# Performance work log

Hardware: AMD Instinct MI355X
Metric: run time of the kernel (lower is better)

The kernel has to match this reference:

```python
import jax, jax.numpy as jnp
import numpy as np

BETA = 0.25  # commitment loss coefficient


def setup_inputs() -> dict:
    key = jax.random.key(0)
    kx, kc = jax.random.split(key)
    # x: [B, T, D] latents; codebooks: [M, K, D] (equal K per level -> stacked)
    x = jax.random.normal(kx, (64, 1024, 256), dtype=jnp.float32)
    # small init akin to RandomUniform(-1/K, 1/K)
    codebooks = jax.random.normal(kc, (4, 1024, 256), dtype=jnp.float32) * (1.0 / 1024.0)
    return {"x": x, "codebooks": codebooks}


def reference(x, codebooks):
    """Residual VQ forward (inference path: no EMA state update).

    Returns (y, commit_loss): y = x + stop_grad(sum_l q_l - x) (straight-through),
    commit_loss = beta * sum_l mean((stop_grad(q_l) - r_l)^2).
    """
    D = x.shape[-1]
    M = codebooks.shape[0]
    flat = x.reshape(-1, D)                      # [N, D]
    residual = flat
    q_sum = jnp.zeros_like(flat)
    commit = jnp.zeros((), dtype=x.dtype)
    for lvl in range(M):                         # M is small & fixed (4)
        cb = codebooks[lvl]                      # [K, D]
        # squared L2 distances: ||r||^2 + ||e||^2 - 2 r.e^T
        r2 = jnp.sum(residual * residual, axis=1, keepdims=True)   # [N, 1]
        e2 = jnp.sum(cb * cb, axis=1)                               # [K]
        dist = r2 + e2 - 2.0 * jnp.matmul(residual, cb.T)           # [N, K]
        idx = jnp.argmin(dist, axis=1)                              # [N]
        q = jnp.take(cb, idx, axis=0)                               # [N, D]
        q_st = jax.lax.stop_gradient(q)
        commit = commit + BETA * jnp.mean((q_st - residual) ** 2)
        q_sum = q_sum + q
        residual = residual - q_st
    y_flat = flat + jax.lax.stop_gradient(q_sum - flat)
    return y_flat.reshape(x.shape), commit
```

## Files before the change

kernel.cpp:

```cpp
#include <hip/hip_runtime.h>

#define DIM 256
#define KCODES 1024
#define LEVELS 4
#define CHUNK 64
#define NCHUNK 16
#define TOKB 128
#define NTOK 65536
#define NELEM (NTOK * DIM)

typedef _Float16 h8 __attribute__((ext_vector_type(8)));
typedef _Float16 h4 __attribute__((ext_vector_type(4)));
typedef _Float16 h2 __attribute__((ext_vector_type(2)));
typedef float f4 __attribute__((ext_vector_type(4)));
typedef unsigned int u32;

__device__ __forceinline__ void gload16(const void* g, void* l) {
  __builtin_amdgcn_global_load_lds(
      (const __attribute__((address_space(1))) void*)g,
      (__attribute__((address_space(3))) void*)l, 16, 0, 0);
}

__device__ __forceinline__ float sq8(h8 r, float acc) {
#if __has_builtin(__builtin_amdgcn_fdot2)
  #pragma unroll
  for (int j = 0; j < 4; ++j) {
    h2 p = {r[2 * j], r[2 * j + 1]};
    acc = __builtin_amdgcn_fdot2(p, p, acc, false);
  }
#else
  #pragma unroll
  for (int j = 0; j < 8; ++j) { float v = (float)r[j]; acc += v * v; }
#endif
  return acc;
}

__global__ __launch_bounds__(256) void rvq_prep(const float* __restrict__ cb,
                                                _Float16* __restrict__ cb16,
                                                float* __restrict__ e2p,
                                                float* __restrict__ out) {
  if (blockIdx.x == 0 && threadIdx.x == 0) out[NELEM] = 0.0f;
  const int row = blockIdx.x * 4 + (threadIdx.x >> 6);
  const int lane = threadIdx.x & 63;
  const float* src = cb + (size_t)row * DIM + lane * 4;
  f4 v = *(const f4*)src;
  h4 hv;
  hv[0] = (_Float16)v[0]; hv[1] = (_Float16)v[1];
  hv[2] = (_Float16)v[2]; hv[3] = (_Float16)v[3];
  *(h4*)(cb16 + (size_t)row * DIM + lane * 4) = hv;
  float s = v[0]*v[0] + v[1]*v[1] + v[2]*v[2] + v[3]*v[3];
  #pragma unroll
  for (int off = 32; off; off >>= 1) s += __shfl_xor(s, off, 64);
  if (lane == 0) e2p[row] = 0.25f - 0.5f * s;
}

__global__ __launch_bounds__(256, 2) void rvq_main(
    const float* __restrict__ x, const float* __restrict__ cb32,
    const _Float16* __restrict__ cb16, const float* __restrict__ e2p,
    float* __restrict__ out) {
  __shared__ __attribute__((aligned(16))) _Float16 clds[2][CHUNK * DIM];
  __shared__ float e2_lds[KCODES];
  __shared__ __attribute__((aligned(16))) int idx_hist[TOKB][4];
  __shared__ float r2_sh[TOKB];
  __shared__ float csum_sh[4];

  const int tid = threadIdx.x;
  const int wave = tid >> 6, lane = tid & 63;
  const int col = lane & 15, quad = lane >> 4;
  const int Llo = lane & 31, Lhi = lane >> 5;

  int soff[8], rdoff[8];
  #pragma unroll
  for (int i = 0; i < 8; ++i) {
    const int rl = wave * 16 + 2 * i + Lhi;
    soff[i] = rl * 512 + ((Llo ^ (rl & 7)) << 4);
  }
  #pragma unroll
  for (int kk = 0; kk < 8; ++kk)
    rdoff[kk] = (((kk * 4 + quad) ^ (col & 7)) << 4);

  const char* cb16b = (const char*)cb16;
  {
    char* ldst = (char*)&clds[0][0] + wave * 8192;
    #pragma unroll
    for (int i = 0; i < 8; ++i) gload16(cb16b + soff[i], ldst + i * 1024);
  }

  h8 af[2][8];
  float r2p[2] = {0.f, 0.f};
  const size_t tok0 = (size_t)blockIdx.x * TOKB + wave * 32;
  #pragma unroll
  for (int mt = 0; mt < 2; ++mt) {
    const float* xr = x + (tok0 + mt * 16 + col) * DIM + quad * 8;
    #pragma unroll
    for (int kk = 0; kk < 8; ++kk) {
      f4 a = *(const f4*)(xr + kk * 32);
      f4 b = *(const f4*)(xr + kk * 32 + 4);
      h8 h;
      #pragma unroll
      for (int j = 0; j < 4; ++j) { h[j] = (_Float16)a[j]; h[4 + j] = (_Float16)b[j]; }
      af[mt][kk] = h;
      r2p[mt] = sq8(h, r2p[mt]);
    }
  }

  float commit_acc = 0.f;

  for (int lvl = 0; lvl < LEVELS; ++lvl) {
    #pragma unroll
    for (int mt = 0; mt < 2; ++mt) {
      float s = r2p[mt];
      s += __shfl_xor(s, 16, 64);
      s += __shfl_xor(s, 32, 64);
      if (quad == 0) r2_sh[wave * 32 + mt * 16 + col] = s;
    }
    *(f4*)&e2_lds[tid * 4] = *(const f4*)(e2p + (lvl << 10) + tid * 4);

    u32 best[2][4];
    #pragma unroll
    for (int mt = 0; mt < 2; ++mt)
      #pragma unroll
      for (int i = 0; i < 4; ++i) best[mt][i] = 0u;

    for (int c = 0; c < NCHUNK; ++c) {
      __syncthreads();
      {
        const int gn = lvl * NCHUNK + c + 1;
        const char* gsrc = cb16b + ((size_t)(gn < 64 ? gn : 63) << 15);
        char* ldst = (char*)&clds[(c + 1) & 1][0] + wave * 8192;
        #pragma unroll
        for (int i = 0; i < 8; ++i) gload16(gsrc + soff[i], ldst + i * 1024);
      }

      const char* cbuf = (const char*)&clds[c & 1][0];
      #pragma unroll
      for (int nt = 0; nt < 4; ++nt) {
        const int code0 = c * 64 + nt * 16;
        const float e2v = e2_lds[code0 + col];
        f4 acc0 = {e2v, e2v, e2v, e2v};
        f4 acc1 = acc0;
        const char* bptr = cbuf + (nt * 16 + col) * 512;
        #pragma unroll
        for (int kk = 0; kk < 8; ++kk) {
          h8 b = *(const h8*)(bptr + rdoff[kk]);
          acc0 = __builtin_amdgcn_mfma_f32_16x16x32_f16(af[0][kk], b, acc0, 0, 0, 0);
          acc1 = __builtin_amdgcn_mfma_f32_16x16x32_f16(af[1][kk], b, acc1, 0, 0, 0);
        }
        const u32 invc = (u32)(code0 + col) ^ 1023u;
        #pragma unroll
        for (int i = 0; i < 4; ++i) {
          u32 p0 = (__float_as_uint(acc0[i]) & 0xFFFFFC00u) | invc;
          if (p0 > best[0][i]) best[0][i] = p0;
          u32 p1 = (__float_as_uint(acc1[i]) & 0xFFFFFC00u) | invc;
          if (p1 > best[1][i]) best[1][i] = p1;
        }
      }
    }

    #pragma unroll
    for (int mt = 0; mt < 2; ++mt)
      #pragma unroll
      for (int i = 0; i < 4; ++i) {
        u32 b = best[mt][i];
        #pragma unroll
        for (int off = 1; off < 16; off <<= 1) {
          u32 o = __shfl_xor(b, off, 16);
          if (o > b) b = o;
        }
        best[mt][i] = b;
      }

    if (col == 0) {
      #pragma unroll
      for (int mt = 0; mt < 2; ++mt)
        #pragma unroll
        for (int i = 0; i < 4; ++i) {
          const u32 p = best[mt][i];
          const int code = (int)((p & 1023u) ^ 1023u);
          const int t = wave * 32 + mt * 16 + quad * 4 + i;
          idx_hist[t][lvl] = code;
          const float sc = __uint_as_float(p & 0xFFFFFC00u) - 0.25f;
          commit_acc += r2_sh[t] - 2.0f * sc;
        }
    }
    __syncthreads();

    if (lvl < LEVELS - 1) {
      r2p[0] = 0.f; r2p[1] = 0.f;
      #pragma unroll
      for (int mt = 0; mt < 2; ++mt) {
        const int qidx = idx_hist[wave * 32 + mt * 16 + col][lvl];
        const _Float16* qr = cb16 + (((size_t)lvl << 10) + qidx) * DIM + quad * 8;
        #pragma unroll
        for (int kk = 0; kk < 8; ++kk) {
          h8 q = *(const h8*)(qr + kk * 32);
          h8 r = af[mt][kk] - q;
          af[mt][kk] = r;
          r2p[mt] = sq8(r, r2p[mt]);
        }
      }
    }
  }

  float* yblk = out + (size_t)blockIdx.x * (TOKB * DIM);
  #pragma unroll 4
  for (int it = 0; it < 32; ++it) {
    const int f = it * 1024 + tid * 4;
    const int t = f >> 8;
    const int d = f & 255;
    const int4 qi = *(const int4*)&idx_hist[t][0];
    f4 q0 = *(const f4*)(cb32 + (size_t)qi.x * DIM + d);
    f4 q1 = *(const f4*)(cb32 + (size_t)(1024 + qi.y) * DIM + d);
    f4 q2 = *(const f4*)(cb32 + (size_t)(2048 + qi.z) * DIM + d);
    f4 q3 = *(const f4*)(cb32 + (size_t)(3072 + qi.w) * DIM + d);
    f4 y = (q0 + q1) + (q2 + q3);
    *(f4*)(yblk + f) = y;
  }

  #pragma unroll
  for (int off = 1; off < 64; off <<= 1) commit_acc += __shfl_xor(commit_acc, off, 64);
  if (lane == 0) csum_sh[wave] = commit_acc;
  __syncthreads();
  if (tid == 0) {
    const float tot = csum_sh[0] + csum_sh[1] + csum_sh[2] + csum_sh[3];
    atomicAdd(out + NELEM, tot * (0.25f / 16777216.0f));
  }
}

extern "C" void kernel_launch(void* const* d_in, const int* in_sizes, int n_in,
                              void* d_out, int out_size, void* d_ws, size_t ws_size,
                              hipStream_t stream) {
  const float* x = (const float*)d_in[0];
  const float* cb = (const float*)d_in[1];
  float* out = (float*)d_out;
  _Float16* cb16 = (_Float16*)d_ws;
  float* e2p = (float*)((char*)d_ws + (size_t)LEVELS * KCODES * DIM * sizeof(_Float16));

  rvq_prep<<<(LEVELS * KCODES) / 4, 256, 0, stream>>>(cb, cb16, e2p, out);
  rvq_main<<<NTOK / TOKB, 256, 0, stream>>>(x, cb, cb16, e2p, out);
}
```

Baseline: 248.7 us.

## Switch to 32x32x16 MFMA tiles with two waves covering 64 tokens each

Replaces the 16x16x32 MFMA tiling with 32x32x16 MFMA, so each wave computes 64 tokens against 32-code tiles, and halves the block to 128 threads (2 waves) with launch bounds of 1 block. Larger MFMA tiles raise arithmetic intensity per LDS fragment read and cut LDS traffic per FLOP. In exchange, register use grows (32 A fragments and 32 best values per thread), occupancy drops, and each wave loads twice as much of the codebook chunk.

```diff
diff --git a/kernel.cpp b/kernel.cpp
--- a/kernel.cpp
+++ b/kernel.cpp
@@ -13,6 +13,7 @@
 typedef _Float16 h4 __attribute__((ext_vector_type(4)));
 typedef _Float16 h2 __attribute__((ext_vector_type(2)));
 typedef float f4 __attribute__((ext_vector_type(4)));
+typedef float f16v __attribute__((ext_vector_type(16)));
 typedef unsigned int u32;
 
 __device__ __forceinline__ void gload16(const void* g, void* l) {
@@ -54,7 +55,7 @@
   if (lane == 0) e2p[row] = 0.25f - 0.5f * s;
 }
 
-__global__ __launch_bounds__(256, 2) void rvq_main(
+__global__ __launch_bounds__(128, 1) void rvq_main(
     const float* __restrict__ x, const float* __restrict__ cb32,
     const _Float16* __restrict__ cb16, const float* __restrict__ e2p,
     float* __restrict__ out) {
@@ -62,40 +63,40 @@
   __shared__ float e2_lds[KCODES];
   __shared__ __attribute__((aligned(16))) int idx_hist[TOKB][4];
   __shared__ float r2_sh[TOKB];
-  __shared__ float csum_sh[4];
+  __shared__ float csum_sh[2];
 
   const int tid = threadIdx.x;
   const int wave = tid >> 6, lane = tid & 63;
-  const int col = lane & 15, quad = lane >> 4;
-  const int Llo = lane & 31, Lhi = lane >> 5;
-
-  int soff[8], rdoff[8];
-  #pragma unroll
-  for (int i = 0; i < 8; ++i) {
-    const int rl = wave * 16 + 2 * i + Lhi;
-    soff[i] = rl * 512 + ((Llo ^ (rl & 7)) << 4);
-  }
-  #pragma unroll
-  for (int kk = 0; kk < 8; ++kk)
-    rdoff[kk] = (((kk * 4 + quad) ^ (col & 7)) << 4);
+  const int col = lane & 31, Lhi = lane >> 5;
+
+  int soff[16];
+  #pragma unroll
+  for (int i = 0; i < 16; ++i) {
+    const int rl = wave * 32 + 2 * i + Lhi;
+    soff[i] = rl * 512 + ((col ^ (rl & 7)) << 4);
+  }
+  int swz4[4];
+  #pragma unroll
+  for (int m = 0; m < 4; ++m)
+    swz4[m] = (((((m << 1) | Lhi) ^ col) & 7) << 4);
 
   const char* cb16b = (const char*)cb16;
   {
-    char* ldst = (char*)&clds[0][0] + wave * 8192;
-    #pragma unroll
-    for (int i = 0; i < 8; ++i) gload16(cb16b + soff[i], ldst + i * 1024);
-  }
-
-  h8 af[2][8];
+    char* ldst = (char*)&clds[0][0] + wave * 16384;
+    #pragma unroll
+    for (int i = 0; i < 16; ++i) gload16(cb16b + soff[i], ldst + i * 1024);
+  }
+
+  h8 af[2][16];
   float r2p[2] = {0.f, 0.f};
-  const size_t tok0 = (size_t)blockIdx.x * TOKB + wave * 32;
+  const size_t tok0 = (size_t)blockIdx.x * TOKB + wave * 64;
   #pragma unroll
   for (int mt = 0; mt < 2; ++mt) {
-    const float* xr = x + (tok0 + mt * 16 + col) * DIM + quad * 8;
-    #pragma unroll
-    for (int kk = 0; kk < 8; ++kk) {
-      f4 a = *(const f4*)(xr + kk * 32);
-      f4 b = *(const f4*)(xr + kk * 32 + 4);
+    const float* xr = x + (tok0 + mt * 32 + col) * DIM + Lhi * 8;
+    #pragma unroll
+    for (int kk = 0; kk < 16; ++kk) {
+      f4 a = *(const f4*)(xr + kk * 16);
+      f4 b = *(const f4*)(xr + kk * 16 + 4);
       h8 h;
       #pragma unroll
       for (int j = 0; j < 4; ++j) { h[j] = (_Float16)a[j]; h[4 + j] = (_Float16)b[j]; }
@@ -109,46 +110,45 @@
   for (int lvl = 0; lvl < LEVELS; ++lvl) {
     #pragma unroll
     for (int mt = 0; mt < 2; ++mt) {
-      float s = r2p[mt];
-      s += __shfl_xor(s, 16, 64);
-      s += __shfl_xor(s, 32, 64);
-      if (quad == 0) r2_sh[wave * 32 + mt * 16 + col] = s;
-    }
-    *(f4*)&e2_lds[tid * 4] = *(const f4*)(e2p + (lvl << 10) + tid * 4);
-
-    u32 best[2][4];
+      float s = r2p[mt] + __shfl_xor(r2p[mt], 32, 64);
+      if (Lhi == 0) r2_sh[wave * 64 + mt * 32 + col] = s;
+    }
+    *(f4*)&e2_lds[tid * 8] = *(const f4*)(e2p + (lvl << 10) + tid * 8);
+    *(f4*)&e2_lds[tid * 8 + 4] = *(const f4*)(e2p + (lvl << 10) + tid * 8 + 4);
+
+    u32 best[2][16];
     #pragma unroll
     for (int mt = 0; mt < 2; ++mt)
       #pragma unroll
-      for (int i = 0; i < 4; ++i) best[mt][i] = 0u;
+      for (int i = 0; i < 16; ++i) best[mt][i] = 0u;
 
     for (int c = 0; c < NCHUNK; ++c) {
       __syncthreads();
       {
         const int gn = lvl * NCHUNK + c + 1;
         const char* gsrc = cb16b + ((size_t)(gn < 64 ? gn : 63) << 15);
-        char* ldst = (char*)&clds[(c + 1) & 1][0] + wave * 8192;
-        #pragma unroll
-        for (int i = 0; i < 8; ++i) gload16(gsrc + soff[i], ldst + i * 1024);
-      }
-
-      const char* cbuf = (const char*)&clds[c & 1][0];
-      #pragma unroll
-      for (int nt = 0; nt < 4; ++nt) {
-        const int code0 = c * 64 + nt * 16;
+        char* ldst = (char*)&clds[(c + 1) & 1][0] + wave * 16384;
+        #pragma unroll
+        for (int i = 0; i < 16; ++i) gload16(gsrc + soff[i], ldst + i * 1024);
+      }
+
+      const char* cbuf = (const char*)&clds[c & 1][0] + col * 512;
+      #pragma unroll
+      for (int nt = 0; nt < 2; ++nt) {
+        const int code0 = c * 64 + nt * 32;
         const float e2v = e2_lds[code0 + col];
-        f4 acc0 = {e2v, e2v, e2v, e2v};
-        f4 acc1 = acc0;
-        const char* bptr = cbuf + (nt * 16 + col) * 512;
-        #pragma unroll
-        for (int kk = 0; kk < 8; ++kk) {
-          h8 b = *(const h8*)(bptr + rdoff[kk]);
-          acc0 = __builtin_amdgcn_mfma_f32_16x16x32_f16(af[0][kk], b, acc0, 0, 0, 0);
-          acc1 = __builtin_amdgcn_mfma_f32_16x16x32_f16(af[1][kk], b, acc1, 0, 0, 0);
+        f16v acc0, acc1;
+        #pragma unroll
+        for (int i = 0; i < 16; ++i) { acc0[i] = e2v; acc1[i] = e2v; }
+        #pragma unroll
+        for (int kk = 0; kk < 16; ++kk) {
+          h8 b = *(const h8*)(cbuf + nt * 16384 + swz4[kk & 3] + ((kk >> 2) << 7));
+          acc0 = __builtin_amdgcn_mfma_f32_32x32x16_f16(af[0][kk], b, acc0, 0, 0, 0);
+          acc1 = __builtin_amdgcn_mfma_f32_32x32x16_f16(af[1][kk], b, acc1, 0, 0, 0);
         }
         const u32 invc = (u32)(code0 + col) ^ 1023u;
         #pragma unroll
-        for (int i = 0; i < 4; ++i) {
+        for (int i = 0; i < 16; ++i) {
           u32 p0 = (__float_as_uint(acc0[i]) & 0xFFFFFC00u) | invc;
           if (p0 > best[0][i]) best[0][i] = p0;
           u32 p1 = (__float_as_uint(acc1[i]) & 0xFFFFFC00u) | invc;
@@ -160,11 +160,11 @@
     #pragma unroll
     for (int mt = 0; mt < 2; ++mt)
       #pragma unroll
-      for (int i = 0; i < 4; ++i) {
+      for (int i = 0; i < 16; ++i) {
         u32 b = best[mt][i];
         #pragma unroll
-        for (int off = 1; off < 16; off <<= 1) {
-          u32 o = __shfl_xor(b, off, 16);
+        for (int off = 1; off < 32; off <<= 1) {
+          u32 o = __shfl_xor(b, off, 32);
           if (o > b) b = o;
         }
         best[mt][i] = b;
@@ -174,10 +174,10 @@
       #pragma unroll
       for (int mt = 0; mt < 2; ++mt)
         #pragma unroll
-        for (int i = 0; i < 4; ++i) {
+        for (int i = 0; i < 16; ++i) {
           const u32 p = best[mt][i];
           const int code = (int)((p & 1023u) ^ 1023u);
-          const int t = wave * 32 + mt * 16 + quad * 4 + i;
+          const int t = wave * 64 + mt * 32 + (i & 3) + 8 * (i >> 2) + 4 * Lhi;
           idx_hist[t][lvl] = code;
           const float sc = __uint_as_float(p & 0xFFFFFC00u) - 0.25f;
           commit_acc += r2_sh[t] - 2.0f * sc;
@@ -189,11 +189,11 @@
       r2p[0] = 0.f; r2p[1] = 0.f;
       #pragma unroll
       for (int mt = 0; mt < 2; ++mt) {
-        const int qidx = idx_hist[wave * 32 + mt * 16 + col][lvl];
-        const _Float16* qr = cb16 + (((size_t)lvl << 10) + qidx) * DIM + quad * 8;
-        #pragma unroll
-        for (int kk = 0; kk < 8; ++kk) {
-          h8 q = *(const h8*)(qr + kk * 32);
+        const int qidx = idx_hist[wave * 64 + mt * 32 + col][lvl];
+        const _Float16* qr = cb16 + (((size_t)lvl << 10) + qidx) * DIM + Lhi * 8;
+        #pragma unroll
+        for (int kk = 0; kk < 16; ++kk) {
+          h8 q = *(const h8*)(qr + kk * 16);
           h8 r = af[mt][kk] - q;
           af[mt][kk] = r;
           r2p[mt] = sq8(r, r2p[mt]);
@@ -204,8 +204,8 @@
 
   float* yblk = out + (size_t)blockIdx.x * (TOKB * DIM);
   #pragma unroll 4
-  for (int it = 0; it < 32; ++it) {
-    const int f = it * 1024 + tid * 4;
+  for (int it = 0; it < 64; ++it) {
+    const int f = it * 512 + tid * 4;
     const int t = f >> 8;
     const int d = f & 255;
     const int4 qi = *(const int4*)&idx_hist[t][0];
@@ -222,7 +222,7 @@
   if (lane == 0) csum_sh[wave] = commit_acc;
   __syncthreads();
   if (tid == 0) {
-    const float tot = csum_sh[0] + csum_sh[1] + csum_sh[2] + csum_sh[3];
+    const float tot = csum_sh[0] + csum_sh[1];
     atomicAdd(out + NELEM, tot * (0.25f / 16777216.0f));
   }
 }
@@ -237,5 +237,5 @@
   float* e2p = (float*)((char*)d_ws + (size_t)LEVELS * KCODES * DIM * sizeof(_Float16));
 
   rvq_prep<<<(LEVELS * KCODES) / 4, 256, 0, stream>>>(cb, cb16, e2p, out);
-  rvq_main<<<NTOK / TOKB, 256, 0, stream>>>(x, cb, cb16, e2p, out);
-}
+  rvq_main<<<NTOK / TOKB, 128, 0, stream>>>(x, cb, cb16, e2p, out);
+}
```

New measurement: 299.4 us. 20.4% more time.
